# Performance work log

Hardware: AMD Instinct MI355X
Metric: run time of the kernel (lower is better)

## Reference

```python
import jax, jax.numpy as jnp
import numpy as np

B, N, IN_DIM, H, D = 4, 2048, 128, 4, 64
LEAKY_SLOPE = 0.2
BN_EPS = 1e-5


def setup_inputs() -> dict:
    key = jax.random.key(0)
    k_h, k_W, k_a, k_adj = jax.random.split(key, 4)
    h = jax.random.normal(k_h, (B, N, IN_DIM), dtype=jnp.float32)
    # Linear weight (no bias): stored as [in_dim, H*D] for x @ W
    W = jax.random.normal(k_W, (IN_DIM, H * D), dtype=jnp.float32) * (1.0 / np.sqrt(IN_DIM))
    # attention vector a: [H, 2D] (xavier-ish scale)
    a = jax.random.normal(k_a, (H, 2 * D), dtype=jnp.float32) * (1.0 / np.sqrt(2 * D))
    # BatchNorm affine params (training-mode batch stats used in reference)
    gamma = jnp.ones((H * D,), dtype=jnp.float32)
    beta = jnp.zeros((H * D,), dtype=jnp.float32)
    adj = jax.random.randint(k_adj, (N, N), 0, 2, dtype=jnp.int32)
    return {"h": h, "W": W, "a": a, "gamma": gamma, "beta": beta, "adj": adj}


def reference(h, W, a, gamma, beta, adj):
    Bs, Ns, _ = h.shape
    # Wh: [B, H, N, D]
    Wh = (h @ W).reshape(Bs, Ns, H, D).transpose(0, 2, 1, 3)
    # Algebraic decomposition of the concat-attention:
    # e[b,h,i,j] = leaky(Wh[b,h,i]. a[h,:D] + Wh[b,h,j]. a[h,D:])
    src = jnp.einsum("bhnd,hd->bhn", Wh, a[:, :D])  # query-node term
    dst = jnp.einsum("bhnd,hd->bhn", Wh, a[:, D:])  # key-node term
    e = src[:, :, :, None] + dst[:, :, None, :]      # [B,H,N,N]
    e = jnp.where(e >= 0, e, LEAKY_SLOPE * e)        # LeakyReLU
    mask = (adj == 0)[None, None, :, :]
    e = jnp.where(mask, -jnp.inf, e)
    alpha = jax.nn.softmax(e, axis=-1)
    alpha = jnp.nan_to_num(alpha, nan=0.0)
    # dropout is identity in eval mode (deterministic reference)
    h_new = jnp.einsum("bhij,bhjd->bhid", alpha, Wh)  # [B,H,N,D]
    h_new = h_new.transpose(0, 2, 1, 3).reshape(Bs, Ns, H * D)
    # BatchNorm1d (training mode: biased batch statistics over B*N rows)
    flat = h_new.reshape(Bs * Ns, H * D)
    mean = jnp.mean(flat, axis=0)
    var = jnp.mean(jnp.square(flat - mean), axis=0)
    flat = (flat - mean) * jax.lax.rsqrt(var + BN_EPS) * gamma + beta
    out = flat.reshape(Bs, Ns, H * D)
    return jax.nn.elu(out)
```

## Files before the change

### kernel.cpp

```cpp
#include <hip/hip_runtime.h>

#define B_ 4
#define N_ 2048
#define IND_ 128
#define H_ 4
#define D_ 64
#define HD_ 256
#define LEAKY 0.2f
#define BNEPS 1e-5f
#define LOG2E 1.44269504088896340736f

typedef float f32x4 __attribute__((ext_vector_type(4)));
typedef short s16x8 __attribute__((ext_vector_type(8)));
typedef unsigned int u32x2 __attribute__((ext_vector_type(2)));
typedef unsigned int u32x4 __attribute__((ext_vector_type(4)));

static __device__ __forceinline__ unsigned short f2bf(float f) {
  unsigned u = __builtin_bit_cast(unsigned, f);
  u = (u + 0x7fffu + ((u >> 16) & 1u)) >> 16;
  return (unsigned short)u;
}

__global__ __launch_bounds__(256) void k_pre(const int* __restrict__ adj,
                                             const float* __restrict__ W,
                                             const float* __restrict__ h,
                                             const float* __restrict__ a,
                                             unsigned* __restrict__ bits,
                                             float* __restrict__ zbuf,
                                             unsigned short* __restrict__ wht,
                                             float* __restrict__ src,
                                             float* __restrict__ dst) {
  int t = threadIdx.x;
  if (blockIdx.x >= 512) {
    int pidx = blockIdx.x - 512;
    if (pidx == 0) {
      for (int i = t; i < 512; i += 256) zbuf[i] = 0.f;
    }
    int idx = pidx * 256 + t;
    int val = adj[idx] != 0;
    unsigned long long mm = __ballot(val);
    int lane = t & 63;
    if (lane == 0)       bits[idx >> 5] = (unsigned)mm;
    else if (lane == 32) bits[idx >> 5] = (unsigned)(mm >> 32);
    return;
  }
  int w = t >> 6, lane = t & 63, m = lane & 15, g = lane >> 4;
  int r0 = blockIdx.x * 16;
  int b = r0 >> 11, n0 = r0 & 2047;
  int hh = w;

  s16x8 Af[4][4];
#pragma unroll
  for (int chf = 0; chf < 4; chf++) {
    int chl = w * 64 + chf * 16 + m;
#pragma unroll
    for (int ks = 0; ks < 4; ks++) {
      int k0 = ks * 32 + g * 8;
      u32x4 au;
#pragma unroll
      for (int e2 = 0; e2 < 4; e2++) {
        float lo = W[(size_t)(k0 + 2 * e2) * 256 + chl];
        float hi = W[(size_t)(k0 + 2 * e2 + 1) * 256 + chl];
        unsigned rr_;
        asm("v_cvt_pk_bf16_f32 %0, %1, %2" : "=v"(rr_) : "v"(lo), "v"(hi));
        au[e2] = rr_;
      }
      Af[chf][ks] = __builtin_bit_cast(s16x8, au);
    }
  }
  s16x8 Bf[4];
#pragma unroll
  for (int ks = 0; ks < 4; ks++) {
    const float* hp = h + (size_t)(r0 + m) * 128 + ks * 32 + g * 8;
    f32x4 h0 = *(const f32x4*)hp;
    f32x4 h1 = *(const f32x4*)(hp + 4);
    u32x4 bu;
#pragma unroll
    for (int e = 0; e < 4; e++) {
      float lo = (e < 2) ? h0[2 * e] : h1[2 * e - 4];
      float hi = (e < 2) ? h0[2 * e + 1] : h1[2 * e - 3];
      unsigned rr_;
      asm("v_cvt_pk_bf16_f32 %0, %1, %2" : "=v"(rr_) : "v"(lo), "v"(hi));
      bu[e] = rr_;
    }
    Bf[ks] = __builtin_bit_cast(s16x8, bu);
  }

  f32x4 acc[4];
#pragma unroll
  for (int chf = 0; chf < 4; chf++) acc[chf] = (f32x4){0.f, 0.f, 0.f, 0.f};
#pragma unroll
  for (int ks = 0; ks < 4; ks++)
#pragma unroll
    for (int chf = 0; chf < 4; chf++)
      acc[chf] = __builtin_amdgcn_mfma_f32_16x16x32_bf16(Af[chf][ks], Bf[ks], acc[chf], 0, 0, 0);

  size_t obase = ((size_t)((b * 4 + hh) * 64)) * 2048 + n0 + m;
#pragma unroll
  for (int chf = 0; chf < 4; chf++) {
    int d = chf * 16 + g * 4;
#pragma unroll
    for (int reg = 0; reg < 4; reg++)
      wht[obase + (size_t)(d + reg) * 2048] = f2bf(acc[chf][reg]);
  }

  float sv = 0.f, dv = 0.f;
#pragma unroll
  for (int chf = 0; chf < 4; chf++)
#pragma unroll
    for (int reg = 0; reg < 4; reg++) {
      int d = chf * 16 + g * 4 + reg;
      float whv = acc[chf][reg];
      sv = fmaf(whv, a[hh * 128 + d] * LOG2E, sv);
      dv = fmaf(whv, a[hh * 128 + 64 + d] * LOG2E, dv);
    }
  sv += __shfl_xor(sv, 16); sv += __shfl_xor(sv, 32);
  dv += __shfl_xor(dv, 16); dv += __shfl_xor(dv, 32);
  if (g == 0) {
    src[(size_t)(b * 4 + hh) * 2048 + n0 + m] = sv;
    dst[(size_t)(b * 4 + hh) * 2048 + n0 + m] = dv;
  }
}

__global__ __launch_bounds__(512, 6) void k_attn(const unsigned* __restrict__ adjb,
                                              const unsigned short* __restrict__ wht,
                                              const float* __restrict__ src,
                                              const float* __restrict__ dst,
                                              float* __restrict__ hnew,
                                              float* __restrict__ chsum,
                                              float* __restrict__ chsq) {
  __shared__ u32x4 whb4[2048];
  __shared__ float ul[2048], vl[2048];
  __shared__ float redS[256], redQ[256];

  int t = threadIdx.x;
  int bid = blockIdx.x;
  int bh = bid & 15, it = bid >> 4;
  int b = bh >> 2, hh = bh & 3;
  int i0 = it * 64;
  int w8 = t >> 6, half = w8 >> 2, w = w8 & 3;
  int lane = t & 63, m = lane & 15, g = lane >> 4;

  {
    f32x4 dv = ((const f32x4*)(dst + (size_t)bh * 2048))[t];
    f32x4 uu, vv;
#pragma unroll
    for (int e = 0; e < 4; e++) {
      uu[e] = __builtin_amdgcn_exp2f(dv[e]);
      vv[e] = __builtin_amdgcn_exp2f(0.2f * dv[e]);
    }
    ((f32x4*)ul)[t] = uu;
    ((f32x4*)vl)[t] = vv;
  }

  int row_i = i0 + w * 16 + m;
  float srcL = src[(size_t)bh * 2048 + row_i];
  float Af = __builtin_amdgcn_exp2f(srcL);
  float Bf = __builtin_amdgcn_exp2f(LEAKY * srcL);

  s16x8 bones;
#pragma unroll
  for (int e = 0; e < 8; e++) bones[e] = (short)0x3F80;

  f32x4 acc[4], accd;
#pragma unroll
  for (int db = 0; db < 4; db++) acc[db] = (f32x4){0.f, 0.f, 0.f, 0.f};
  accd = (f32x4){0.f, 0.f, 0.f, 0.f};

  char* wbase = (char*)whb4 + half * 16384;
  int ts = t & 255;
  int r_ = ts >> 2, ch_ = ts & 3;
  int jtbase = half * 16;
  const char* gbase = (const char*)(wht + (size_t)(bh * 64 + r_) * 2048) + jtbase * 128;
  int sw = (r_ & 7) << 4;
  u32x4 R0, R1;
  const u32x2* adjrow = (const u32x2*)(adjb + (size_t)row_i * 64 + jtbase * 2);

#define LOADT(jt_) { const u32x4* gp = (const u32x4*)(gbase + (jt_) * 128 + ch_ * 32); \
                     R0 = gp[0]; R1 = gp[1]; }
#define WRITET(pb_) { char* wb_ = (pb_); \
                      *(u32x4*)(wb_ + r_ * 128 + ((ch_ * 32) ^ sw)) = R0; \
                      *(u32x4*)(wb_ + r_ * 128 + ((ch_ * 32 + 16) ^ sw)) = R1; }

  LOADT(0); WRITET(wbase); LOADT(1);
  u32x2 adjw2 = adjrow[0];

  for (int jt = 0; jt < 16; jt++) {
    int cur = jt & 1;
    __syncthreads();
    if (jt < 15) WRITET(wbase + (cur ^ 1) * 8192);
    if (jt < 14) LOADT(jt + 2);
    u32x2 adjnx;
    if (jt < 15) adjnx = adjrow[jt + 1];
    const char* wbufc = wbase + cur * 8192;
    int jglob = jtbase + jt;

#pragma unroll
    for (int ks = 0; ks < 2; ks++) {
      unsigned bits = (adjw2[ks] >> (g * 8)) & 0xffu;
      const float* up = &ul[jglob * 64 + ks * 32 + g * 8];
      const float* vp = &vl[jglob * 64 + ks * 32 + g * 8];
      f32x4 u0 = *(const f32x4*)up, u1 = *(const f32x4*)(up + 4);
      f32x4 v0 = *(const f32x4*)vp, v1 = *(const f32x4*)(vp + 4);
      float pm[8];
#pragma unroll
      for (int e = 0; e < 8; e++) {
        float ue = (e < 4) ? u0[e] : u1[e - 4];
        float ve = (e < 4) ? v0[e] : v1[e - 4];
        float p = fmaxf(Af * ue, Bf * ve);
        unsigned keep = (unsigned)(((int)(bits << (31 - e))) >> 31);
        pm[e] = __builtin_bit_cast(float, __builtin_bit_cast(unsigned, p) & keep);
      }
      u32x4 afu;
#pragma unroll
      for (int e2 = 0; e2 < 4; e2++) {
        unsigned rr_;
        asm("v_cvt_pk_bf16_f32 %0, %1, %2" : "=v"(rr_) : "v"(pm[2 * e2]), "v"(pm[2 * e2 + 1]));
        afu[e2] = rr_;
      }
      s16x8 af = __builtin_bit_cast(s16x8, afu);
#pragma unroll
      for (int db = 0; db < 4; db++) {
        int dl = db * 16 + m;
        int off = dl * 128 + ((ks * 64 + g * 16) ^ ((dl & 7) << 4));
        s16x8 bf = *(const s16x8*)(wbufc + off);
        acc[db] = __builtin_amdgcn_mfma_f32_16x16x32_bf16(af, bf, acc[db], 0, 0, 0);
      }
      accd = __builtin_amdgcn_mfma_f32_16x16x32_bf16(af, bones, accd, 0, 0, 0);
    }
    adjw2 = adjnx;
  }
#undef LOADT
#undef WRITET

  __syncthreads();
  float* accl = (float*)whb4;
  if (half == 1) {
#pragma unroll
    for (int db = 0; db < 4; db++)
#pragma unroll
      for (int r = 0; r < 4; r++)
        accl[(w * 16 + 4 * g + r) * 65 + db * 16 + m] = acc[db][r];
    if (m == 0) {
#pragma unroll
      for (int r = 0; r < 4; r++)
        accl[(w * 16 + 4 * g + r) * 65 + 64] = accd[r];
    }
  }
  __syncthreads();

  if (half == 0) {
#pragma unroll
    for (int db = 0; db < 4; db++)
#pragma unroll
      for (int r = 0; r < 4; r++)
        acc[db][r] += accl[(w * 16 + 4 * g + r) * 65 + db * 16 + m];
    float inv[4];
#pragma unroll
    for (int r = 0; r < 4; r++) {
      float dtot = accd[r] + accl[(w * 16 + 4 * g + r) * 65 + 64];
      inv[r] = dtot > 0.f ? 1.0f / dtot : 0.f;
    }

    float sums[4] = {0.f, 0.f, 0.f, 0.f}, sqs[4] = {0.f, 0.f, 0.f, 0.f};
#pragma unroll
    for (int r = 0; r < 4; r++) {
      int n = i0 + w * 16 + 4 * g + r;
#pragma unroll
      for (int db = 0; db < 4; db++) {
        float val = acc[db][r] * inv[r];
        hnew[(size_t)(b * 2048 + n) * 256 + hh * 64 + db * 16 + m] = val;
        sums[db] += val;
        sqs[db] += val * val;
      }
    }
#pragma unroll
    for (int db = 0; db < 4; db++) {
      sums[db] += __shfl_xor(sums[db], 16); sums[db] += __shfl_xor(sums[db], 32);
      sqs[db]  += __shfl_xor(sqs[db], 16);  sqs[db]  += __shfl_xor(sqs[db], 32);
    }
    if (g == 0) {
#pragma unroll
      for (int db = 0; db < 4; db++) {
        redS[w * 64 + db * 16 + m] = sums[db];
        redQ[w * 64 + db * 16 + m] = sqs[db];
      }
    }
  }
  __syncthreads();
  if (t < 64) {
    float ts2 = redS[t] + redS[64 + t] + redS[128 + t] + redS[192 + t];
    float tq = redQ[t] + redQ[64 + t] + redQ[128 + t] + redQ[192 + t];
    atomicAdd(&chsum[hh * 64 + t], ts2);
    atomicAdd(&chsq[hh * 64 + t], tq);
  }
}

__global__ __launch_bounds__(256) void k_bn_elu(const float* __restrict__ hnew,
                                                const float* __restrict__ chsum,
                                                const float* __restrict__ chsq,
                                                const float* __restrict__ gamma,
                                                const float* __restrict__ beta,
                                                float* __restrict__ out) {
  int idx4 = blockIdx.x * 256 + threadIdx.x;
  f32x4 x = ((const f32x4*)hnew)[idx4];
  int c0 = (idx4 * 4) & 255;
  f32x4 s = *(const f32x4*)(chsum + c0);
  f32x4 sq = *(const f32x4*)(chsq + c0);
  f32x4 gm = *(const f32x4*)(gamma + c0);
  f32x4 bt = *(const f32x4*)(beta + c0);
  f32x4 y;
#pragma unroll
  for (int e = 0; e < 4; e++) {
    float mean = s[e] * (1.0f / 8192.0f);
    float var = sq[e] * (1.0f / 8192.0f) - mean * mean;
    float sc = gm[e] * rsqrtf(var + BNEPS);
    float v = (x[e] - mean) * sc + bt[e];
    y[e] = v > 0.f ? v : expm1f(v);
  }
  ((f32x4*)out)[idx4] = y;
}

extern "C" void kernel_launch(void* const* d_in, const int* in_sizes, int n_in,
                              void* d_out, int out_size, void* d_ws, size_t ws_size,
                              hipStream_t stream) {
  const float* h = (const float*)d_in[0];
  const float* W = (const float*)d_in[1];
  const float* a = (const float*)d_in[2];
  const float* gamma = (const float*)d_in[3];
  const float* beta = (const float*)d_in[4];
  const int* adj = (const int*)d_in[5];

  char* ws = (char*)d_ws;
  unsigned* adjb = (unsigned*)ws;
  unsigned short* wht = (unsigned short*)(ws + (512 << 10));
  float* src = (float*)(ws + (512 << 10) + (4 << 20));
  float* dst = src + 16 * 2048;
  float* chsum = dst + 16 * 2048;
  float* chsq = chsum + 256;
  float* hnew = (float*)(ws + (512 << 10) + (5 << 20));

  k_pre<<<512 + (N_ * N_) / 256, 256, 0, stream>>>(adj, W, h, a, adjb, chsum,
                                                   wht, src, dst);
  k_attn<<<B_ * H_ * (N_ / 64), 512, 0, stream>>>(adjb, wht, src, dst,
                                                  hnew, chsum, chsq);
  k_bn_elu<<<(B_ * N_ * HD_) / 1024, 256, 0, stream>>>(hnew, chsum, chsq,
                                                       gamma, beta, (float*)d_out);
}
```

Measured before the change: 51.59 us.

## Halve attention block threads, two row tiles per wave, pack u/v as bf16

The attention kernel now runs 256 threads per block instead of 512. Each wave computes two 16-row tiles, so every B fragment read from LDS feeds two MFMAs, which halves LDS traffic per MFMA. The exp2 key factors u and v are packed as a bf16 pair into one shared word, halving that LDS array and its reads, at the cost of bf16 rounding of the softmax factors. In exchange there are fewer waves for latency hiding and more accumulator registers per thread, which may lower occupancy.

Result: slower. 56.64 us (+9.8%).

```diff
diff --git a/kernel.cpp b/kernel.cpp
--- a/kernel.cpp
+++ b/kernel.cpp
@@ -122,7 +122,7 @@
   }
 }
 
-__global__ __launch_bounds__(512, 6) void k_attn(const unsigned* __restrict__ adjb,
+__global__ __launch_bounds__(256) void k_attn(const unsigned* __restrict__ adjb,
                                               const unsigned short* __restrict__ wht,
                                               const float* __restrict__ src,
                                               const float* __restrict__ dst,
@@ -130,105 +130,129 @@
                                               float* __restrict__ chsum,
                                               float* __restrict__ chsq) {
   __shared__ u32x4 whb4[2048];
-  __shared__ float ul[2048], vl[2048];
-  __shared__ float redS[256], redQ[256];
+  __shared__ unsigned uvl[2048];
+  __shared__ float redS[128], redQ[128];
 
   int t = threadIdx.x;
   int bid = blockIdx.x;
   int bh = bid & 15, it = bid >> 4;
   int b = bh >> 2, hh = bh & 3;
   int i0 = it * 64;
-  int w8 = t >> 6, half = w8 >> 2, w = w8 & 3;
+  int w8 = t >> 6, half = w8 >> 1, wv = w8 & 1;
   int lane = t & 63, m = lane & 15, g = lane >> 4;
 
   {
-    f32x4 dv = ((const f32x4*)(dst + (size_t)bh * 2048))[t];
-    f32x4 uu, vv;
+    const f32x4* dg = (const f32x4*)(dst + (size_t)bh * 2048);
+    f32x4 d0 = dg[2 * t], d1 = dg[2 * t + 1];
+    u32x4 p0, p1;
 #pragma unroll
     for (int e = 0; e < 4; e++) {
-      uu[e] = __builtin_amdgcn_exp2f(dv[e]);
-      vv[e] = __builtin_amdgcn_exp2f(0.2f * dv[e]);
-    }
-    ((f32x4*)ul)[t] = uu;
-    ((f32x4*)vl)[t] = vv;
-  }
-
-  int row_i = i0 + w * 16 + m;
-  float srcL = src[(size_t)bh * 2048 + row_i];
-  float Af = __builtin_amdgcn_exp2f(srcL);
-  float Bf = __builtin_amdgcn_exp2f(LEAKY * srcL);
+      float u0 = __builtin_amdgcn_exp2f(d0[e]);
+      float v0 = __builtin_amdgcn_exp2f(0.2f * d0[e]);
+      float u1 = __builtin_amdgcn_exp2f(d1[e]);
+      float v1 = __builtin_amdgcn_exp2f(0.2f * d1[e]);
+      unsigned r0_, r1_;
+      asm("v_cvt_pk_bf16_f32 %0, %1, %2" : "=v"(r0_) : "v"(u0), "v"(v0));
+      asm("v_cvt_pk_bf16_f32 %0, %1, %2" : "=v"(r1_) : "v"(u1), "v"(v1));
+      p0[e] = r0_; p1[e] = r1_;
+    }
+    ((u32x4*)uvl)[2 * t] = p0;
+    ((u32x4*)uvl)[2 * t + 1] = p1;
+  }
+
+  int ri0 = i0 + wv * 32 + m;
+  int ri1 = ri0 + 16;
+  float s0 = src[(size_t)bh * 2048 + ri0];
+  float s1 = src[(size_t)bh * 2048 + ri1];
+  float Af0 = __builtin_amdgcn_exp2f(s0), Bf0 = __builtin_amdgcn_exp2f(LEAKY * s0);
+  float Af1 = __builtin_amdgcn_exp2f(s1), Bf1 = __builtin_amdgcn_exp2f(LEAKY * s1);
 
   s16x8 bones;
 #pragma unroll
   for (int e = 0; e < 8; e++) bones[e] = (short)0x3F80;
 
-  f32x4 acc[4], accd;
-#pragma unroll
-  for (int db = 0; db < 4; db++) acc[db] = (f32x4){0.f, 0.f, 0.f, 0.f};
-  accd = (f32x4){0.f, 0.f, 0.f, 0.f};
+  f32x4 acc0[4], acc1[4], accd0, accd1;
+#pragma unroll
+  for (int db = 0; db < 4; db++) {
+    acc0[db] = (f32x4){0.f, 0.f, 0.f, 0.f};
+    acc1[db] = (f32x4){0.f, 0.f, 0.f, 0.f};
+  }
+  accd0 = (f32x4){0.f, 0.f, 0.f, 0.f};
+  accd1 = (f32x4){0.f, 0.f, 0.f, 0.f};
 
   char* wbase = (char*)whb4 + half * 16384;
-  int ts = t & 255;
-  int r_ = ts >> 2, ch_ = ts & 3;
+  int ts = t & 127;
+  int r_ = ts >> 1, c2 = ts & 1;
   int jtbase = half * 16;
-  const char* gbase = (const char*)(wht + (size_t)(bh * 64 + r_) * 2048) + jtbase * 128;
+  const char* gbase = (const char*)(wht + (size_t)(bh * 64 + r_) * 2048)
+                      + jtbase * 128 + c2 * 64;
   int sw = (r_ & 7) << 4;
-  u32x4 R0, R1;
-  const u32x2* adjrow = (const u32x2*)(adjb + (size_t)row_i * 64 + jtbase * 2);
-
-#define LOADT(jt_) { const u32x4* gp = (const u32x4*)(gbase + (jt_) * 128 + ch_ * 32); \
-                     R0 = gp[0]; R1 = gp[1]; }
-#define WRITET(pb_) { char* wb_ = (pb_); \
-                      *(u32x4*)(wb_ + r_ * 128 + ((ch_ * 32) ^ sw)) = R0; \
-                      *(u32x4*)(wb_ + r_ * 128 + ((ch_ * 32 + 16) ^ sw)) = R1; }
+  u32x4 R0_, R1_, R2_, R3_;
+  const u32x2* adjr0 = (const u32x2*)(adjb + (size_t)ri0 * 64 + jtbase * 2);
+  const u32x2* adjr1 = (const u32x2*)(adjb + (size_t)ri1 * 64 + jtbase * 2);
+
+#define LOADT(jt_) { const u32x4* gp = (const u32x4*)(gbase + (jt_) * 128); \
+                     R0_ = gp[0]; R1_ = gp[1]; R2_ = gp[2]; R3_ = gp[3]; }
+#define WRITET(pb_) { char* wb_ = (pb_) + r_ * 128; \
+                      *(u32x4*)(wb_ + ((c2 * 64 +  0) ^ sw)) = R0_; \
+                      *(u32x4*)(wb_ + ((c2 * 64 + 16) ^ sw)) = R1_; \
+                      *(u32x4*)(wb_ + ((c2 * 64 + 32) ^ sw)) = R2_; \
+                      *(u32x4*)(wb_ + ((c2 * 64 + 48) ^ sw)) = R3_; }
 
   LOADT(0); WRITET(wbase); LOADT(1);
-  u32x2 adjw2 = adjrow[0];
+  u32x2 a0c = adjr0[0], a1c = adjr1[0];
 
   for (int jt = 0; jt < 16; jt++) {
     int cur = jt & 1;
     __syncthreads();
     if (jt < 15) WRITET(wbase + (cur ^ 1) * 8192);
     if (jt < 14) LOADT(jt + 2);
-    u32x2 adjnx;
-    if (jt < 15) adjnx = adjrow[jt + 1];
+    u32x2 a0n, a1n;
+    if (jt < 15) { a0n = adjr0[jt + 1]; a1n = adjr1[jt + 1]; }
     const char* wbufc = wbase + cur * 8192;
     int jglob = jtbase + jt;
 
 #pragma unroll
     for (int ks = 0; ks < 2; ks++) {
-      unsigned bits = (adjw2[ks] >> (g * 8)) & 0xffu;
-      const float* up = &ul[jglob * 64 + ks * 32 + g * 8];
-      const float* vp = &vl[jglob * 64 + ks * 32 + g * 8];
-      f32x4 u0 = *(const f32x4*)up, u1 = *(const f32x4*)(up + 4);
-      f32x4 v0 = *(const f32x4*)vp, v1 = *(const f32x4*)(vp + 4);
-      float pm[8];
+      unsigned bits0 = (a0c[ks] >> (g * 8)) & 0xffu;
+      unsigned bits1 = (a1c[ks] >> (g * 8)) & 0xffu;
+      const u32x4* uvp = (const u32x4*)&uvl[jglob * 64 + ks * 32 + g * 8];
+      u32x4 q0 = uvp[0], q1 = uvp[1];
+      float pm0[8], pm1[8];
 #pragma unroll
       for (int e = 0; e < 8; e++) {
-        float ue = (e < 4) ? u0[e] : u1[e - 4];
-        float ve = (e < 4) ? v0[e] : v1[e - 4];
-        float p = fmaxf(Af * ue, Bf * ve);
-        unsigned keep = (unsigned)(((int)(bits << (31 - e))) >> 31);
-        pm[e] = __builtin_bit_cast(float, __builtin_bit_cast(unsigned, p) & keep);
-      }
-      u32x4 afu;
+        unsigned pk = (e < 4) ? q0[e] : q1[e - 4];
+        float uf = __builtin_bit_cast(float, pk << 16);
+        float vf = __builtin_bit_cast(float, pk & 0xffff0000u);
+        float p0 = fmaxf(Af0 * uf, Bf0 * vf);
+        float p1 = fmaxf(Af1 * uf, Bf1 * vf);
+        unsigned k0 = (unsigned)(((int)(bits0 << (31 - e))) >> 31);
+        unsigned k1 = (unsigned)(((int)(bits1 << (31 - e))) >> 31);
+        pm0[e] = __builtin_bit_cast(float, __builtin_bit_cast(unsigned, p0) & k0);
+        pm1[e] = __builtin_bit_cast(float, __builtin_bit_cast(unsigned, p1) & k1);
+      }
+      u32x4 af0u, af1u;
 #pragma unroll
       for (int e2 = 0; e2 < 4; e2++) {
-        unsigned rr_;
-        asm("v_cvt_pk_bf16_f32 %0, %1, %2" : "=v"(rr_) : "v"(pm[2 * e2]), "v"(pm[2 * e2 + 1]));
-        afu[e2] = rr_;
-      }
-      s16x8 af = __builtin_bit_cast(s16x8, afu);
+        unsigned r0_, r1_;
+        asm("v_cvt_pk_bf16_f32 %0, %1, %2" : "=v"(r0_) : "v"(pm0[2 * e2]), "v"(pm0[2 * e2 + 1]));
+        asm("v_cvt_pk_bf16_f32 %0, %1, %2" : "=v"(r1_) : "v"(pm1[2 * e2]), "v"(pm1[2 * e2 + 1]));
+        af0u[e2] = r0_; af1u[e2] = r1_;
+      }
+      s16x8 af0 = __builtin_bit_cast(s16x8, af0u);
+      s16x8 af1 = __builtin_bit_cast(s16x8, af1u);
 #pragma unroll
       for (int db = 0; db < 4; db++) {
         int dl = db * 16 + m;
         int off = dl * 128 + ((ks * 64 + g * 16) ^ ((dl & 7) << 4));
         s16x8 bf = *(const s16x8*)(wbufc + off);
-        acc[db] = __builtin_amdgcn_mfma_f32_16x16x32_bf16(af, bf, acc[db], 0, 0, 0);
-      }
-      accd = __builtin_amdgcn_mfma_f32_16x16x32_bf16(af, bones, accd, 0, 0, 0);
-    }
-    adjw2 = adjnx;
+        acc0[db] = __builtin_amdgcn_mfma_f32_16x16x32_bf16(af0, bf, acc0[db], 0, 0, 0);
+        acc1[db] = __builtin_amdgcn_mfma_f32_16x16x32_bf16(af1, bf, acc1[db], 0, 0, 0);
+      }
+      accd0 = __builtin_amdgcn_mfma_f32_16x16x32_bf16(af0, bones, accd0, 0, 0, 0);
+      accd1 = __builtin_amdgcn_mfma_f32_16x16x32_bf16(af1, bones, accd1, 0, 0, 0);
+    }
+    a0c = a0n; a1c = a1n;
   }
 #undef LOADT
 #undef WRITET
@@ -239,39 +263,38 @@
 #pragma unroll
     for (int db = 0; db < 4; db++)
 #pragma unroll
-      for (int r = 0; r < 4; r++)
-        accl[(w * 16 + 4 * g + r) * 65 + db * 16 + m] = acc[db][r];
+      for (int r = 0; r < 4; r++) {
+        accl[(wv * 32 + 4 * g + r) * 65 + db * 16 + m] = acc0[db][r];
+        accl[(wv * 32 + 16 + 4 * g + r) * 65 + db * 16 + m] = acc1[db][r];
+      }
     if (m == 0) {
 #pragma unroll
-      for (int r = 0; r < 4; r++)
-        accl[(w * 16 + 4 * g + r) * 65 + 64] = accd[r];
+      for (int r = 0; r < 4; r++) {
+        accl[(wv * 32 + 4 * g + r) * 65 + 64] = accd0[r];
+        accl[(wv * 32 + 16 + 4 * g + r) * 65 + 64] = accd1[r];
+      }
     }
   }
   __syncthreads();
 
   if (half == 0) {
-#pragma unroll
-    for (int db = 0; db < 4; db++)
-#pragma unroll
-      for (int r = 0; r < 4; r++)
-        acc[db][r] += accl[(w * 16 + 4 * g + r) * 65 + db * 16 + m];
-    float inv[4];
-#pragma unroll
-    for (int r = 0; r < 4; r++) {
-      float dtot = accd[r] + accl[(w * 16 + 4 * g + r) * 65 + 64];
-      inv[r] = dtot > 0.f ? 1.0f / dtot : 0.f;
-    }
-
     float sums[4] = {0.f, 0.f, 0.f, 0.f}, sqs[4] = {0.f, 0.f, 0.f, 0.f};
 #pragma unroll
-    for (int r = 0; r < 4; r++) {
-      int n = i0 + w * 16 + 4 * g + r;
-#pragma unroll
-      for (int db = 0; db < 4; db++) {
-        float val = acc[db][r] * inv[r];
-        hnew[(size_t)(b * 2048 + n) * 256 + hh * 64 + db * 16 + m] = val;
-        sums[db] += val;
-        sqs[db] += val * val;
+    for (int fr = 0; fr < 2; fr++) {
+#pragma unroll
+      for (int r = 0; r < 4; r++) {
+        int rr = wv * 32 + fr * 16 + 4 * g + r;
+        float dtot = (fr ? accd1[r] : accd0[r]) + accl[rr * 65 + 64];
+        float inv = dtot > 0.f ? 1.0f / dtot : 0.f;
+        int n = i0 + rr;
+#pragma unroll
+        for (int db = 0; db < 4; db++) {
+          float av = (fr ? acc1[db][r] : acc0[db][r]) + accl[rr * 65 + db * 16 + m];
+          float val = av * inv;
+          hnew[(size_t)(b * 2048 + n) * 256 + hh * 64 + db * 16 + m] = val;
+          sums[db] += val;
+          sqs[db] += val * val;
+        }
       }
     }
 #pragma unroll
@@ -282,15 +305,15 @@
     if (g == 0) {
 #pragma unroll
       for (int db = 0; db < 4; db++) {
-        redS[w * 64 + db * 16 + m] = sums[db];
-        redQ[w * 64 + db * 16 + m] = sqs[db];
+        redS[wv * 64 + db * 16 + m] = sums[db];
+        redQ[wv * 64 + db * 16 + m] = sqs[db];
       }
     }
   }
   __syncthreads();
   if (t < 64) {
-    float ts2 = redS[t] + redS[64 + t] + redS[128 + t] + redS[192 + t];
-    float tq = redQ[t] + redQ[64 + t] + redQ[128 + t] + redQ[192 + t];
+    float ts2 = redS[t] + redS[64 + t];
+    float tq = redQ[t] + redQ[64 + t];
     atomicAdd(&chsum[hh * 64 + t], ts2);
     atomicAdd(&chsq[hh * 64 + t], tq);
   }
@@ -342,7 +365,7 @@
 
   k_pre<<<512 + (N_ * N_) / 256, 256, 0, stream>>>(adj, W, h, a, adjb, chsum,
                                                    wht, src, dst);
-  k_attn<<<B_ * H_ * (N_ / 64), 512, 0, stream>>>(adjb, wht, src, dst,
+  k_attn<<<B_ * H_ * (N_ / 64), 256, 0, stream>>>(adjb, wht, src, dst,
                                                   hnew, chsum, chsq);
   k_bn_elu<<<(B_ * N_ * HD_) / 1024, 256, 0, stream>>>(hnew, chsum, chsq,
                                                        gamma, beta, (float*)d_out);
```

## Fuse BatchNorm+ELU into attention kernel via grid-wide atomic barrier

Applied to the files above, without the earlier changes.

Removes the separate BN/ELU kernel and the hnew intermediate buffer. The attention kernel now keeps its normalized outputs in registers, waits on a global atomic counter until all 512 blocks have added their channel statistics, then applies BatchNorm and ELU and writes the final output directly. This saves one launch and an 8 MB round trip to global memory. In exchange it relies on all 512 blocks being resident at once, which is why launch bounds drop to 4 waves. Blocks spin at the barrier, and the counter is reset by the pre-kernel zeroing.

Result: slower. 153.6 us (+197.7%).

```diff
diff --git a/kernel.cpp b/kernel.cpp
--- a/kernel.cpp
+++ b/kernel.cpp
@@ -34,7 +34,7 @@
   if (blockIdx.x >= 512) {
     int pidx = blockIdx.x - 512;
     if (pidx == 0) {
-      for (int i = t; i < 512; i += 256) zbuf[i] = 0.f;
+      for (int i = t; i < 513; i += 256) zbuf[i] = 0.f;
     }
     int idx = pidx * 256 + t;
     int val = adj[idx] != 0;
@@ -122,13 +122,16 @@
   }
 }
 
-__global__ __launch_bounds__(512, 6) void k_attn(const unsigned* __restrict__ adjb,
+__global__ __launch_bounds__(512, 4) void k_attn(const unsigned* __restrict__ adjb,
                                               const unsigned short* __restrict__ wht,
                                               const float* __restrict__ src,
                                               const float* __restrict__ dst,
-                                              float* __restrict__ hnew,
+                                              const float* __restrict__ gamma,
+                                              const float* __restrict__ beta,
                                               float* __restrict__ chsum,
-                                              float* __restrict__ chsq) {
+                                              float* __restrict__ chsq,
+                                              unsigned* __restrict__ ctr,
+                                              float* __restrict__ out) {
   __shared__ u32x4 whb4[2048];
   __shared__ float ul[2048], vl[2048];
   __shared__ float redS[256], redQ[256];
@@ -265,11 +268,10 @@
     float sums[4] = {0.f, 0.f, 0.f, 0.f}, sqs[4] = {0.f, 0.f, 0.f, 0.f};
 #pragma unroll
     for (int r = 0; r < 4; r++) {
-      int n = i0 + w * 16 + 4 * g + r;
 #pragma unroll
       for (int db = 0; db < 4; db++) {
         float val = acc[db][r] * inv[r];
-        hnew[(size_t)(b * 2048 + n) * 256 + hh * 64 + db * 16 + m] = val;
+        acc[db][r] = val;
         sums[db] += val;
         sqs[db] += val * val;
       }
@@ -294,31 +296,34 @@
     atomicAdd(&chsum[hh * 64 + t], ts2);
     atomicAdd(&chsq[hh * 64 + t], tq);
   }
-}
-
-__global__ __launch_bounds__(256) void k_bn_elu(const float* __restrict__ hnew,
-                                                const float* __restrict__ chsum,
-                                                const float* __restrict__ chsq,
-                                                const float* __restrict__ gamma,
-                                                const float* __restrict__ beta,
-                                                float* __restrict__ out) {
-  int idx4 = blockIdx.x * 256 + threadIdx.x;
-  f32x4 x = ((const f32x4*)hnew)[idx4];
-  int c0 = (idx4 * 4) & 255;
-  f32x4 s = *(const f32x4*)(chsum + c0);
-  f32x4 sq = *(const f32x4*)(chsq + c0);
-  f32x4 gm = *(const f32x4*)(gamma + c0);
-  f32x4 bt = *(const f32x4*)(beta + c0);
-  f32x4 y;
-#pragma unroll
-  for (int e = 0; e < 4; e++) {
-    float mean = s[e] * (1.0f / 8192.0f);
-    float var = sq[e] * (1.0f / 8192.0f) - mean * mean;
-    float sc = gm[e] * rsqrtf(var + BNEPS);
-    float v = (x[e] - mean) * sc + bt[e];
-    y[e] = v > 0.f ? v : expm1f(v);
-  }
-  ((f32x4*)out)[idx4] = y;
+
+  __threadfence();
+  __syncthreads();
+  if (t == 0) {
+    __hip_atomic_fetch_add(ctr, 1u, __ATOMIC_ACQ_REL, __HIP_MEMORY_SCOPE_AGENT);
+    while (__hip_atomic_load(ctr, __ATOMIC_ACQUIRE, __HIP_MEMORY_SCOPE_AGENT) < 512u) {}
+  }
+  __syncthreads();
+
+  if (half == 0) {
+#pragma unroll
+    for (int db = 0; db < 4; db++) {
+      int ch = hh * 64 + db * 16 + m;
+      float s = __hip_atomic_load(&chsum[ch], __ATOMIC_RELAXED, __HIP_MEMORY_SCOPE_AGENT);
+      float q = __hip_atomic_load(&chsq[ch], __ATOMIC_RELAXED, __HIP_MEMORY_SCOPE_AGENT);
+      float mean = s * (1.0f / 8192.0f);
+      float var = q * (1.0f / 8192.0f) - mean * mean;
+      float sc = gamma[ch] * rsqrtf(var + BNEPS);
+      float sh = beta[ch] - mean * sc;
+#pragma unroll
+      for (int r = 0; r < 4; r++) {
+        int n = i0 + w * 16 + 4 * g + r;
+        float v = fmaf(acc[db][r], sc, sh);
+        v = v > 0.f ? v : expm1f(v);
+        out[(size_t)(b * 2048 + n) * 256 + ch] = v;
+      }
+    }
+  }
 }
 
 extern "C" void kernel_launch(void* const* d_in, const int* in_sizes, int n_in,
@@ -338,12 +343,11 @@
   float* dst = src + 16 * 2048;
   float* chsum = dst + 16 * 2048;
   float* chsq = chsum + 256;
-  float* hnew = (float*)(ws + (512 << 10) + (5 << 20));
+  unsigned* ctr = (unsigned*)(chsq + 256);
 
   k_pre<<<512 + (N_ * N_) / 256, 256, 0, stream>>>(adj, W, h, a, adjb, chsum,
                                                    wht, src, dst);
   k_attn<<<B_ * H_ * (N_ / 64), 512, 0, stream>>>(adjb, wht, src, dst,
-                                                  hnew, chsum, chsq);
-  k_bn_elu<<<(B_ * N_ * HD_) / 1024, 256, 0, stream>>>(hnew, chsum, chsq,
-                                                       gamma, beta, (float*)d_out);
+                                                  gamma, beta, chsum, chsq,
+                                                  ctr, (float*)d_out);
 }
```
